# Kernel optimization log

Hardware: AMD Instinct MI355X
Metric: run time of the kernel (lower is better)

The kernel has to match this reference:

```python
import jax, jax.numpy as jnp
import numpy as np

N_NODES = 50000
N_EDGES = 800000
D_IN = 64
D_OUT = 64


def setup_inputs() -> dict:
    key = jax.random.key(0)
    k1, k2, k3, k4, k5 = jax.random.split(key, 5)
    x = jax.random.normal(k1, (N_NODES, D_IN), dtype=jnp.float32)
    senders = jax.random.randint(k2, (N_EDGES,), 0, N_NODES, dtype=jnp.int32)
    receivers = jax.random.randint(k3, (N_EDGES,), 0, N_NODES, dtype=jnp.int32)
    # eqx.nn.Linear params: weight [out, in], bias [out]
    weight = jax.random.normal(k4, (D_OUT, D_IN), dtype=jnp.float32) / np.sqrt(D_IN)
    bias = jax.random.normal(k5, (D_OUT,), dtype=jnp.float32) * 0.01
    return {"x": x, "senders": senders, "receivers": receivers, "weight": weight, "bias": bias}


def reference(x, senders, receivers, weight, bias):
    n = x.shape[0]
    # jraph.GraphConvolution applies update_node_fn (the Linear) FIRST
    h = x @ weight.T + bias  # [N, D_OUT]
    # add self edges
    self_idx = jnp.arange(n, dtype=senders.dtype)
    cs = jnp.concatenate([senders, self_idx])
    cr = jnp.concatenate([receivers, self_idx])
    ones = jnp.ones(cs.shape, dtype=h.dtype)
    sender_deg = jax.ops.segment_sum(ones, cs, num_segments=n)
    receiver_deg = jax.ops.segment_sum(ones, cr, num_segments=n)
    # symmetric normalization: D^{-1/2} A D^{-1/2}
    h = h * jax.lax.rsqrt(jnp.maximum(sender_deg, 1.0))[:, None]
    h = jax.ops.segment_sum(h[cs], cr, num_segments=n)  # gather -> scatter-add
    h = h * jax.lax.rsqrt(jnp.maximum(receiver_deg, 1.0))[:, None]
    return jax.nn.leaky_relu(h)  # default negative_slope=0.01
```

## Files before the change

kernel.cpp:

```cpp
#include <hip/hip_runtime.h>

#define N_NODES 50000
#define N_EDGES 800000
#define D 64
#define NB 196
#define BSZ 256
#define NSLICE 256
#define SLICE_I4 784
#define E4 (N_EDGES / 4)
#define CAP 52
#define CELLW (NB * CAP)

__device__ __forceinline__ ushort f2bf(float f) {
    unsigned u = __float_as_uint(f);
    unsigned r = u + 0x7fffu + ((u >> 16) & 1u);
    return (ushort)(r >> 16);
}
__device__ __forceinline__ void acc8(const uint4 a, float* acc) {
    acc[0] += __uint_as_float(a.x << 16);
    acc[1] += __uint_as_float(a.x & 0xffff0000u);
    acc[2] += __uint_as_float(a.y << 16);
    acc[3] += __uint_as_float(a.y & 0xffff0000u);
    acc[4] += __uint_as_float(a.z << 16);
    acc[5] += __uint_as_float(a.z & 0xffff0000u);
    acc[6] += __uint_as_float(a.w << 16);
    acc[7] += __uint_as_float(a.w & 0xffff0000u);
}

__global__ __launch_bounds__(1024) void part1_kernel(
        const int* __restrict__ s, const int* __restrict__ r,
        unsigned* __restrict__ prc, unsigned char* __restrict__ psc,
        int* __restrict__ rcnt, int* __restrict__ scnt) {
    __shared__ unsigned lprc[CELLW];
    __shared__ unsigned char lpsc[CELLW];
    __shared__ int rcur[NB], scur[NB];
    const int tid = threadIdx.x, sl = blockIdx.x;
    for (int i = tid; i < NB; i += 1024) { rcur[i] = 0; scur[i] = 0; }
    __syncthreads();

    int e4 = sl * SLICE_I4 + tid;
    if (tid < SLICE_I4 && e4 < E4) {
        int4 rv = ((const int4*)r)[e4];
        int4 sv = ((const int4*)s)[e4];
        int ri[4] = {rv.x, rv.y, rv.z, rv.w};
        int si[4] = {sv.x, sv.y, sv.z, sv.w};
        #pragma unroll
        for (int k = 0; k < 4; ++k) {
            int b = ri[k] >> 8;
            int pos = atomicAdd(&rcur[b], 1);
            if (pos < CAP)
                lprc[b * CAP + pos] = ((unsigned)(ri[k] & 255) << 16) | (unsigned)si[k];
            int bs = si[k] >> 8;
            int pos2 = atomicAdd(&scur[bs], 1);
            if (pos2 < CAP)
                lpsc[bs * CAP + pos2] = (unsigned char)(si[k] & 255);
        }
    }
    __syncthreads();

    for (int i = tid; i < NB; i += 1024) {
        rcnt[sl * NB + i] = min(rcur[i], CAP);
        scnt[sl * NB + i] = min(scur[i], CAP);
    }
    uint4* gp = (uint4*)(prc + (size_t)sl * CELLW);
    const uint4* lp = (const uint4*)lprc;
    for (int i = tid; i < CELLW / 4; i += 1024) gp[i] = lp[i];
    uint4* gq = (uint4*)(psc + (size_t)sl * CELLW);
    const uint4* lq = (const uint4*)lpsc;
    for (int i = tid; i < CELLW / 16; i += 1024) gq[i] = lq[i];
}

__global__ __launch_bounds__(256, 4) void post_kernel(
        const unsigned* __restrict__ prc, const unsigned char* __restrict__ psc,
        const int* __restrict__ rcnt, const int* __restrict__ scnt,
        int* __restrict__ rowoff, ushort* __restrict__ csr16,
        const float* __restrict__ x, const float* __restrict__ w,
        const float* __restrict__ bias, ushort* __restrict__ h16) {
    __shared__ int sc[256];
    __shared__ int h4[BSZ];
    __shared__ float wlds[64 * 68];
    __shared__ float xlds[64 * 68];
    __shared__ float slds[BSZ];
    __shared__ float blds[64];
    const int tid = threadIdx.x;

    if (blockIdx.x >= NB) {
        const int b = blockIdx.x - NB;
        h4[tid] = 0;
        if (tid < 64) blds[tid] = bias[tid];
        __syncthreads();
        {
            int sl = tid;
            int c = scnt[sl * NB + b];
            const unsigned char* cell = psc + (size_t)sl * CELLW + (size_t)b * CAP;
            for (int i = 0; i < c; ++i) atomicAdd(&h4[cell[i]], 1);
        }
        __syncthreads();
        slds[tid] = rsqrtf((float)(h4[tid] + 1));
        #pragma unroll
        for (int q = 0; q < 4; ++q) {
            int idx = q * 256 + tid;
            int o = idx >> 4, k4 = idx & 15;
            float4 wv = ((const float4*)w)[idx];
            *(float4*)&wlds[o * 68 + k4 * 4] = wv;
        }
        __syncthreads();

        const int t15 = tid & 15;
        const int g = tid >> 4;
        for (int tile = 0; tile < 4; ++tile) {
            const int nb = b * BSZ + tile * 64;
            #pragma unroll
            for (int q = 0; q < 4; ++q) {
                int idx = q * 256 + tid;
                int nl = idx >> 4, k4 = idx & 15;
                int n = nb + nl;
                float4 xv = (n < N_NODES) ? ((const float4*)x)[n * 16 + k4]
                                          : make_float4(0.f, 0.f, 0.f, 0.f);
                *(float4*)&xlds[nl * 68 + k4 * 4] = xv;
            }
            __syncthreads();

            float acc[4][4];
            #pragma unroll
            for (int i = 0; i < 4; ++i)
                #pragma unroll
                for (int j = 0; j < 4; ++j) acc[i][j] = 0.f;

            #pragma unroll 2
            for (int k4 = 0; k4 < 16; ++k4) {
                float4 wv0 = *(const float4*)&wlds[(t15     ) * 68 + k4 * 4];
                float4 wv1 = *(const float4*)&wlds[(t15 + 16) * 68 + k4 * 4];
                float4 wv2 = *(const float4*)&wlds[(t15 + 32) * 68 + k4 * 4];
                float4 wv3 = *(const float4*)&wlds[(t15 + 48) * 68 + k4 * 4];
                #pragma unroll
                for (int i = 0; i < 4; ++i) {
                    float4 xv = *(const float4*)&xlds[(g * 4 + i) * 68 + k4 * 4];
                    acc[i][0] += xv.x * wv0.x + xv.y * wv0.y + xv.z * wv0.z + xv.w * wv0.w;
                    acc[i][1] += xv.x * wv1.x + xv.y * wv1.y + xv.z * wv1.z + xv.w * wv1.w;
                    acc[i][2] += xv.x * wv2.x + xv.y * wv2.y + xv.z * wv2.z + xv.w * wv2.w;
                    acc[i][3] += xv.x * wv3.x + xv.y * wv3.y + xv.z * wv3.z + xv.w * wv3.w;
                }
            }

            #pragma unroll
            for (int i = 0; i < 4; ++i) {
                int nl = g * 4 + i;
                int n = nb + nl;
                if (n < N_NODES) {
                    float scl = slds[tile * 64 + nl];
                    h16[n * D + t15     ] = f2bf((acc[i][0] + blds[t15     ]) * scl);
                    h16[n * D + t15 + 16] = f2bf((acc[i][1] + blds[t15 + 16]) * scl);
                    h16[n * D + t15 + 32] = f2bf((acc[i][2] + blds[t15 + 32]) * scl);
                    h16[n * D + t15 + 48] = f2bf((acc[i][3] + blds[t15 + 48]) * scl);
                }
            }
            __syncthreads();
        }
        return;
    }

    const int b = blockIdx.x;
    int tot = 0;
    if (tid < NB) {
        for (int sl = 0; sl < NSLICE; ++sl) tot += rcnt[sl * NB + tid];
    }
    sc[tid] = tot;
    __syncthreads();
    for (int o = 1; o < 256; o <<= 1) {
        int u = (tid >= o) ? sc[tid - o] : 0;
        __syncthreads();
        sc[tid] += u;
        __syncthreads();
    }
    const int rb = (b == 0) ? 0 : sc[b - 1];
    __syncthreads();

    h4[tid] = 0;
    __syncthreads();
    {
        int sl = tid;
        int c = rcnt[sl * NB + b];
        const unsigned* cell = prc + (size_t)sl * CELLW + (size_t)b * CAP;
        for (int i = 0; i < c; ++i) atomicAdd(&h4[cell[i] >> 16], 1);
    }
    __syncthreads();

    int v = h4[tid];
    sc[tid] = v;
    __syncthreads();
    for (int o = 1; o < 256; o <<= 1) {
        int u = (tid >= o) ? sc[tid - o] : 0;
        __syncthreads();
        sc[tid] += u;
        __syncthreads();
    }
    int excl = sc[tid] - v;
    int n = b * BSZ + tid;
    if (n < N_NODES) rowoff[n] = rb + excl;
    h4[tid] = rb + excl;
    if (b == NB - 1 && tid == 0) rowoff[N_NODES] = N_EDGES;
    __syncthreads();

    {
        int sl = tid;
        int c = rcnt[sl * NB + b];
        const unsigned* cell = prc + (size_t)sl * CELLW + (size_t)b * CAP;
        for (int i = 0; i < c; ++i) {
            unsigned pw = cell[i];
            int pos = atomicAdd(&h4[pw >> 16], 1);
            csr16[pos] = (ushort)(pw & 0xffffu);
        }
    }
}

__global__ __launch_bounds__(256) void gather_kernel(
        const ushort* __restrict__ h16, const int* __restrict__ rowoff,
        const ushort* __restrict__ csr16, float* __restrict__ out) {
    const int lane = threadIdx.x & 63;
    const int q = lane & 7;
    const int g = lane >> 3;
    const int n = blockIdx.x * 4 + (threadIdx.x >> 6);
    if (n >= N_NODES) return;

    float acc[8];
    #pragma unroll
    for (int k = 0; k < 8; ++k) acc[k] = 0.f;

    const int base = rowoff[n];
    const int cnt = rowoff[n + 1] - base;

    for (int j0 = 0; j0 < cnt; j0 += 64) {
        int m = cnt - j0; if (m > 64) m = 64;
        int my = (lane < m) ? (int)csr16[base + j0 + lane] : 0;
        int t = 0;
        for (; t + 16 <= m; t += 16) {
            int s0 = __shfl(my, t + g);
            int s1 = __shfl(my, t + 8 + g);
            uint4 a = *(const uint4*)&h16[s0 * D + q * 8];
            uint4 b = *(const uint4*)&h16[s1 * D + q * 8];
            acc8(a, acc);
            acc8(b, acc);
        }
        for (; t < m; t += 8) {
            int e = t + g;
            int ee = (e < m) ? e : 0;
            int s0 = __shfl(my, ee);
            if (e < m) {
                uint4 a = *(const uint4*)&h16[s0 * D + q * 8];
                acc8(a, acc);
            }
        }
    }

    #pragma unroll
    for (int k = 0; k < 8; ++k) acc[k] += __shfl_xor(acc[k], 8);
    #pragma unroll
    for (int k = 0; k < 8; ++k) acc[k] += __shfl_xor(acc[k], 16);
    #pragma unroll
    for (int k = 0; k < 8; ++k) acc[k] += __shfl_xor(acc[k], 32);

    uint4 sv = *(const uint4*)&h16[n * D + q * 8];
    acc8(sv, acc);
    float sc = rsqrtf((float)(cnt + 1));
    float o[8];
    #pragma unroll
    for (int k = 0; k < 8; ++k) {
        float vv = acc[k] * sc;
        o[k] = vv > 0.f ? vv : 0.01f * vv;
    }
    if (g == 0) {
        *(float4*)(out + n * D + q * 8)     = make_float4(o[0], o[1], o[2], o[3]);
    } else if (g == 1) {
        *(float4*)(out + n * D + q * 8 + 4) = make_float4(o[4], o[5], o[6], o[7]);
    }
}

extern "C" void kernel_launch(void* const* d_in, const int* in_sizes, int n_in,
                              void* d_out, int out_size, void* d_ws, size_t ws_size,
                              hipStream_t stream) {
    const float* x       = (const float*)d_in[0];
    const int*   senders = (const int*)d_in[1];
    const int*   recvs   = (const int*)d_in[2];
    const float* weight  = (const float*)d_in[3];
    const float* bias    = (const float*)d_in[4];
    float* out = (float*)d_out;

    char* p = (char*)d_ws;
    auto take = [&](size_t bytes) { char* q = p; p += (bytes + 255) & ~(size_t)255; return q; };
    ushort*        h16    = (ushort*)take((size_t)N_NODES * D * 2);
    unsigned*      prc    = (unsigned*)take((size_t)NSLICE * CELLW * 4);
    unsigned char* psc    = (unsigned char*)take((size_t)NSLICE * CELLW);
    int*           rcnt   = (int*)take((size_t)NSLICE * NB * 4);
    int*           scnt   = (int*)take((size_t)NSLICE * NB * 4);
    int*           rowoff = (int*)take((size_t)(N_NODES + 1) * 4);
    ushort*        csr16  = (ushort*)take((size_t)N_EDGES * 2);

    hipLaunchKernelGGL(part1_kernel, dim3(NSLICE), dim3(1024), 0, stream,
                       senders, recvs, prc, psc, rcnt, scnt);
    hipLaunchKernelGGL(post_kernel, dim3(2 * NB), dim3(BSZ), 0, stream,
                       prc, psc, rcnt, scnt, rowoff, csr16,
                       x, weight, bias, h16);
    hipLaunchKernelGGL(gather_kernel, dim3((N_NODES + 3) / 4), dim3(256), 0, stream,
                       h16, rowoff, csr16, out);
}
```

Baseline: 62.61 us.

## Move linear transform into bucketing kernel and apply sender scale in gather

The dense linear layer moves out of the post kernel and runs in extra blocks of the first kernel, so it overlaps with edge bucketing. Because the sender-degree scale is not known at that point, the stored bf16 features are unscaled. The post kernel now writes a per-node scale array, and the gather multiplies each neighbor row by that scale with an FMA. The cost is an extra scale load per edge in the gather and 1024-thread blocks each doing one 64-node tile of the matmul.

```diff
diff --git a/kernel.cpp b/kernel.cpp
--- a/kernel.cpp
+++ b/kernel.cpp
@@ -10,84 +10,134 @@
 #define E4 (N_EDGES / 4)
 #define CAP 52
 #define CELLW (NB * CAP)
+#define LIN_BLK 782
 
 __device__ __forceinline__ ushort f2bf(float f) {
     unsigned u = __float_as_uint(f);
     unsigned r = u + 0x7fffu + ((u >> 16) & 1u);
     return (ushort)(r >> 16);
 }
-__device__ __forceinline__ void acc8(const uint4 a, float* acc) {
-    acc[0] += __uint_as_float(a.x << 16);
-    acc[1] += __uint_as_float(a.x & 0xffff0000u);
-    acc[2] += __uint_as_float(a.y << 16);
-    acc[3] += __uint_as_float(a.y & 0xffff0000u);
-    acc[4] += __uint_as_float(a.z << 16);
-    acc[5] += __uint_as_float(a.z & 0xffff0000u);
-    acc[6] += __uint_as_float(a.w << 16);
-    acc[7] += __uint_as_float(a.w & 0xffff0000u);
-}
-
-__global__ __launch_bounds__(1024) void part1_kernel(
+__device__ __forceinline__ void acc8s(const uint4 a, float s, float* acc) {
+    acc[0] = fmaf(__uint_as_float(a.x << 16),         s, acc[0]);
+    acc[1] = fmaf(__uint_as_float(a.x & 0xffff0000u), s, acc[1]);
+    acc[2] = fmaf(__uint_as_float(a.y << 16),         s, acc[2]);
+    acc[3] = fmaf(__uint_as_float(a.y & 0xffff0000u), s, acc[3]);
+    acc[4] = fmaf(__uint_as_float(a.z << 16),         s, acc[4]);
+    acc[5] = fmaf(__uint_as_float(a.z & 0xffff0000u), s, acc[5]);
+    acc[6] = fmaf(__uint_as_float(a.w << 16),         s, acc[6]);
+    acc[7] = fmaf(__uint_as_float(a.w & 0xffff0000u), s, acc[7]);
+}
+
+__global__ __launch_bounds__(1024) void k1_kernel(
         const int* __restrict__ s, const int* __restrict__ r,
+        const float* __restrict__ x, const float* __restrict__ w,
+        const float* __restrict__ bias,
         unsigned* __restrict__ prc, unsigned char* __restrict__ psc,
-        int* __restrict__ rcnt, int* __restrict__ scnt) {
-    __shared__ unsigned lprc[CELLW];
-    __shared__ unsigned char lpsc[CELLW];
-    __shared__ int rcur[NB], scur[NB];
-    const int tid = threadIdx.x, sl = blockIdx.x;
-    for (int i = tid; i < NB; i += 1024) { rcur[i] = 0; scur[i] = 0; }
-    __syncthreads();
-
-    int e4 = sl * SLICE_I4 + tid;
-    if (tid < SLICE_I4 && e4 < E4) {
-        int4 rv = ((const int4*)r)[e4];
-        int4 sv = ((const int4*)s)[e4];
-        int ri[4] = {rv.x, rv.y, rv.z, rv.w};
-        int si[4] = {sv.x, sv.y, sv.z, sv.w};
-        #pragma unroll
-        for (int k = 0; k < 4; ++k) {
-            int b = ri[k] >> 8;
-            int pos = atomicAdd(&rcur[b], 1);
-            if (pos < CAP)
-                lprc[b * CAP + pos] = ((unsigned)(ri[k] & 255) << 16) | (unsigned)si[k];
-            int bs = si[k] >> 8;
-            int pos2 = atomicAdd(&scur[bs], 1);
-            if (pos2 < CAP)
-                lpsc[bs * CAP + pos2] = (unsigned char)(si[k] & 255);
-        }
-    }
-    __syncthreads();
-
-    for (int i = tid; i < NB; i += 1024) {
-        rcnt[sl * NB + i] = min(rcur[i], CAP);
-        scnt[sl * NB + i] = min(scur[i], CAP);
-    }
-    uint4* gp = (uint4*)(prc + (size_t)sl * CELLW);
-    const uint4* lp = (const uint4*)lprc;
-    for (int i = tid; i < CELLW / 4; i += 1024) gp[i] = lp[i];
-    uint4* gq = (uint4*)(psc + (size_t)sl * CELLW);
-    const uint4* lq = (const uint4*)lpsc;
-    for (int i = tid; i < CELLW / 16; i += 1024) gq[i] = lq[i];
-}
-
-__global__ __launch_bounds__(256, 4) void post_kernel(
+        int* __restrict__ rcnt, int* __restrict__ scnt,
+        ushort* __restrict__ h16u) {
+    __shared__ char smem[52544];
+    const int tid = threadIdx.x;
+
+    if (blockIdx.x < NSLICE) {
+        unsigned* lprc      = (unsigned*)smem;
+        unsigned char* lpsc = (unsigned char*)(smem + 40768);
+        int* rcur           = (int*)(smem + 50960);
+        int* scur           = (int*)(smem + 51744);
+        const int sl = blockIdx.x;
+        for (int i = tid; i < NB; i += 1024) { rcur[i] = 0; scur[i] = 0; }
+        __syncthreads();
+
+        int e4 = sl * SLICE_I4 + tid;
+        if (tid < SLICE_I4 && e4 < E4) {
+            int4 rv = ((const int4*)r)[e4];
+            int4 sv = ((const int4*)s)[e4];
+            int ri[4] = {rv.x, rv.y, rv.z, rv.w};
+            int si[4] = {sv.x, sv.y, sv.z, sv.w};
+            #pragma unroll
+            for (int k = 0; k < 4; ++k) {
+                int b = ri[k] >> 8;
+                int pos = atomicAdd(&rcur[b], 1);
+                if (pos < CAP)
+                    lprc[b * CAP + pos] =
+                        ((unsigned)(ri[k] & 255) << 16) | (unsigned)si[k];
+                int bs = si[k] >> 8;
+                int pos2 = atomicAdd(&scur[bs], 1);
+                if (pos2 < CAP)
+                    lpsc[bs * CAP + pos2] = (unsigned char)(si[k] & 255);
+            }
+        }
+        __syncthreads();
+
+        for (int i = tid; i < NB; i += 1024) {
+            rcnt[sl * NB + i] = min(rcur[i], CAP);
+            scnt[sl * NB + i] = min(scur[i], CAP);
+        }
+        uint4* gp = (uint4*)(prc + (size_t)sl * CELLW);
+        const uint4* lp = (const uint4*)lprc;
+        for (int i = tid; i < CELLW / 4; i += 1024) gp[i] = lp[i];
+        uint4* gq = (uint4*)(psc + (size_t)sl * CELLW);
+        const uint4* lq = (const uint4*)lpsc;
+        for (int i = tid; i < CELLW / 16; i += 1024) gq[i] = lq[i];
+        return;
+    }
+
+    float* wlds = (float*)smem;
+    float* xlds = (float*)(smem + 17408);
+    float* blds = (float*)(smem + 34816);
+    const int tile = blockIdx.x - NSLICE;
+    const int nb = tile * 64;
+
+    {
+        int o = tid >> 4, k4 = tid & 15;
+        float4 wv = ((const float4*)w)[tid];
+        *(float4*)&wlds[o * 68 + k4 * 4] = wv;
+    }
+    if (tid < 64) blds[tid] = bias[tid];
+    {
+        int nl = tid >> 4, k4 = tid & 15;
+        int n = nb + nl;
+        float4 xv = (n < N_NODES) ? ((const float4*)x)[n * 16 + k4]
+                                  : make_float4(0.f, 0.f, 0.f, 0.f);
+        *(float4*)&xlds[nl * 68 + k4 * 4] = xv;
+    }
+    __syncthreads();
+
+    const int nl = tid >> 4;
+    const int t15 = tid & 15;
+    float a0 = 0.f, a1 = 0.f, a2 = 0.f, a3 = 0.f;
+    #pragma unroll 4
+    for (int k4 = 0; k4 < 16; ++k4) {
+        float4 xv = *(const float4*)&xlds[nl * 68 + k4 * 4];
+        float4 w0 = *(const float4*)&wlds[(t15     ) * 68 + k4 * 4];
+        float4 w1 = *(const float4*)&wlds[(t15 + 16) * 68 + k4 * 4];
+        float4 w2 = *(const float4*)&wlds[(t15 + 32) * 68 + k4 * 4];
+        float4 w3 = *(const float4*)&wlds[(t15 + 48) * 68 + k4 * 4];
+        a0 += xv.x * w0.x + xv.y * w0.y + xv.z * w0.z + xv.w * w0.w;
+        a1 += xv.x * w1.x + xv.y * w1.y + xv.z * w1.z + xv.w * w1.w;
+        a2 += xv.x * w2.x + xv.y * w2.y + xv.z * w2.z + xv.w * w2.w;
+        a3 += xv.x * w3.x + xv.y * w3.y + xv.z * w3.z + xv.w * w3.w;
+    }
+    int n = nb + nl;
+    if (n < N_NODES) {
+        h16u[n * D + t15     ] = f2bf(a0 + blds[t15     ]);
+        h16u[n * D + t15 + 16] = f2bf(a1 + blds[t15 + 16]);
+        h16u[n * D + t15 + 32] = f2bf(a2 + blds[t15 + 32]);
+        h16u[n * D + t15 + 48] = f2bf(a3 + blds[t15 + 48]);
+    }
+}
+
+__global__ __launch_bounds__(256) void post_kernel(
         const unsigned* __restrict__ prc, const unsigned char* __restrict__ psc,
         const int* __restrict__ rcnt, const int* __restrict__ scnt,
         int* __restrict__ rowoff, ushort* __restrict__ csr16,
-        const float* __restrict__ x, const float* __restrict__ w,
-        const float* __restrict__ bias, ushort* __restrict__ h16) {
+        float* __restrict__ sscale) {
     __shared__ int sc[256];
     __shared__ int h4[BSZ];
-    __shared__ float wlds[64 * 68];
-    __shared__ float xlds[64 * 68];
-    __shared__ float slds[BSZ];
-    __shared__ float blds[64];
     const int tid = threadIdx.x;
 
     if (blockIdx.x >= NB) {
         const int b = blockIdx.x - NB;
         h4[tid] = 0;
-        if (tid < 64) blds[tid] = bias[tid];
         __syncthreads();
         {
             int sl = tid;
@@ -96,67 +146,8 @@
             for (int i = 0; i < c; ++i) atomicAdd(&h4[cell[i]], 1);
         }
         __syncthreads();
-        slds[tid] = rsqrtf((float)(h4[tid] + 1));
-        #pragma unroll
-        for (int q = 0; q < 4; ++q) {
-            int idx = q * 256 + tid;
-            int o = idx >> 4, k4 = idx & 15;
-            float4 wv = ((const float4*)w)[idx];
-            *(float4*)&wlds[o * 68 + k4 * 4] = wv;
-        }
-        __syncthreads();
-
-        const int t15 = tid & 15;
-        const int g = tid >> 4;
-        for (int tile = 0; tile < 4; ++tile) {
-            const int nb = b * BSZ + tile * 64;
-            #pragma unroll
-            for (int q = 0; q < 4; ++q) {
-                int idx = q * 256 + tid;
-                int nl = idx >> 4, k4 = idx & 15;
-                int n = nb + nl;
-                float4 xv = (n < N_NODES) ? ((const float4*)x)[n * 16 + k4]
-                                          : make_float4(0.f, 0.f, 0.f, 0.f);
-                *(float4*)&xlds[nl * 68 + k4 * 4] = xv;
-            }
-            __syncthreads();
-
-            float acc[4][4];
-            #pragma unroll
-            for (int i = 0; i < 4; ++i)
-                #pragma unroll
-                for (int j = 0; j < 4; ++j) acc[i][j] = 0.f;
-
-            #pragma unroll 2
-            for (int k4 = 0; k4 < 16; ++k4) {
-                float4 wv0 = *(const float4*)&wlds[(t15     ) * 68 + k4 * 4];
-                float4 wv1 = *(const float4*)&wlds[(t15 + 16) * 68 + k4 * 4];
-                float4 wv2 = *(const float4*)&wlds[(t15 + 32) * 68 + k4 * 4];
-                float4 wv3 = *(const float4*)&wlds[(t15 + 48) * 68 + k4 * 4];
-                #pragma unroll
-                for (int i = 0; i < 4; ++i) {
-                    float4 xv = *(const float4*)&xlds[(g * 4 + i) * 68 + k4 * 4];
-                    acc[i][0] += xv.x * wv0.x + xv.y * wv0.y + xv.z * wv0.z + xv.w * wv0.w;
-                    acc[i][1] += xv.x * wv1.x + xv.y * wv1.y + xv.z * wv1.z + xv.w * wv1.w;
-                    acc[i][2] += xv.x * wv2.x + xv.y * wv2.y + xv.z * wv2.z + xv.w * wv2.w;
-                    acc[i][3] += xv.x * wv3.x + xv.y * wv3.y + xv.z * wv3.z + xv.w * wv3.w;
-                }
-            }
-
-            #pragma unroll
-            for (int i = 0; i < 4; ++i) {
-                int nl = g * 4 + i;
-                int n = nb + nl;
-                if (n < N_NODES) {
-                    float scl = slds[tile * 64 + nl];
-                    h16[n * D + t15     ] = f2bf((acc[i][0] + blds[t15     ]) * scl);
-                    h16[n * D + t15 + 16] = f2bf((acc[i][1] + blds[t15 + 16]) * scl);
-                    h16[n * D + t15 + 32] = f2bf((acc[i][2] + blds[t15 + 32]) * scl);
-                    h16[n * D + t15 + 48] = f2bf((acc[i][3] + blds[t15 + 48]) * scl);
-                }
-            }
-            __syncthreads();
-        }
+        int n = b * BSZ + tid;
+        if (n < N_NODES) sscale[n] = rsqrtf((float)(h4[tid] + 1));
         return;
     }
 
@@ -215,8 +206,9 @@
 }
 
 __global__ __launch_bounds__(256) void gather_kernel(
-        const ushort* __restrict__ h16, const int* __restrict__ rowoff,
-        const ushort* __restrict__ csr16, float* __restrict__ out) {
+        const ushort* __restrict__ h16u, const float* __restrict__ sscale,
+        const int* __restrict__ rowoff, const ushort* __restrict__ csr16,
+        float* __restrict__ out) {
     const int lane = threadIdx.x & 63;
     const int q = lane & 7;
     const int g = lane >> 3;
@@ -237,18 +229,20 @@
         for (; t + 16 <= m; t += 16) {
             int s0 = __shfl(my, t + g);
             int s1 = __shfl(my, t + 8 + g);
-            uint4 a = *(const uint4*)&h16[s0 * D + q * 8];
-            uint4 b = *(const uint4*)&h16[s1 * D + q * 8];
-            acc8(a, acc);
-            acc8(b, acc);
+            uint4 a = *(const uint4*)&h16u[s0 * D + q * 8];
+            uint4 b = *(const uint4*)&h16u[s1 * D + q * 8];
+            float c0 = sscale[s0];
+            float c1 = sscale[s1];
+            acc8s(a, c0, acc);
+            acc8s(b, c1, acc);
         }
         for (; t < m; t += 8) {
             int e = t + g;
             int ee = (e < m) ? e : 0;
             int s0 = __shfl(my, ee);
             if (e < m) {
-                uint4 a = *(const uint4*)&h16[s0 * D + q * 8];
-                acc8(a, acc);
+                uint4 a = *(const uint4*)&h16u[s0 * D + q * 8];
+                acc8s(a, sscale[s0], acc);
             }
         }
     }
@@ -260,8 +254,8 @@
     #pragma unroll
     for (int k = 0; k < 8; ++k) acc[k] += __shfl_xor(acc[k], 32);
 
-    uint4 sv = *(const uint4*)&h16[n * D + q * 8];
-    acc8(sv, acc);
+    uint4 sv = *(const uint4*)&h16u[n * D + q * 8];
+    acc8s(sv, sscale[n], acc);
     float sc = rsqrtf((float)(cnt + 1));
     float o[8];
     #pragma unroll
@@ -288,7 +282,8 @@
 
     char* p = (char*)d_ws;
     auto take = [&](size_t bytes) { char* q = p; p += (bytes + 255) & ~(size_t)255; return q; };
-    ushort*        h16    = (ushort*)take((size_t)N_NODES * D * 2);
+    ushort*        h16u   = (ushort*)take((size_t)N_NODES * D * 2);
+    float*         sscale = (float*)take((size_t)N_NODES * 4);
     unsigned*      prc    = (unsigned*)take((size_t)NSLICE * CELLW * 4);
     unsigned char* psc    = (unsigned char*)take((size_t)NSLICE * CELLW);
     int*           rcnt   = (int*)take((size_t)NSLICE * NB * 4);
@@ -296,11 +291,11 @@
     int*           rowoff = (int*)take((size_t)(N_NODES + 1) * 4);
     ushort*        csr16  = (ushort*)take((size_t)N_EDGES * 2);
 
-    hipLaunchKernelGGL(part1_kernel, dim3(NSLICE), dim3(1024), 0, stream,
-                       senders, recvs, prc, psc, rcnt, scnt);
+    hipLaunchKernelGGL(k1_kernel, dim3(NSLICE + LIN_BLK), dim3(1024), 0, stream,
+                       senders, recvs, x, weight, bias,
+                       prc, psc, rcnt, scnt, h16u);
     hipLaunchKernelGGL(post_kernel, dim3(2 * NB), dim3(BSZ), 0, stream,
-                       prc, psc, rcnt, scnt, rowoff, csr16,
-                       x, weight, bias, h16);
+                       prc, psc, rcnt, scnt, rowoff, csr16, sscale);
     hipLaunchKernelGGL(gather_kernel, dim3((N_NODES + 3) / 4), dim3(256), 0, stream,
-                       h16, rowoff, csr16, out);
-}
+                       h16u, sscale, rowoff, csr16, out);
+}
```

Measured after the change: 68.24 us. 9.0% more time.
